# Performance work log

Measured on AMD Instinct MI355X. Metric: run time of the kernel, lower is better.

Reference implementation:

```python
import jax, jax.numpy as jnp
import numpy as np

EMB = 32      # emb_size = input_size // 2
IN = 64       # input_size
H = 128       # hidden_size
OUT = 256     # output_size (byte vocab)
TEMP = 1e-3   # Decoder_lstm.temperature


def _bytes(x):
    # x: [N] nonneg int32 -> [N, 4] big-endian bytes (vectorized get_bytes_2d)
    shifts = jnp.array([24, 16, 8, 0], dtype=x.dtype)
    return (x[:, None] >> shifts) & 0xFF


def _embed4(tables, byts):
    # tables: [4, 256, EMB]; byts: [N, 4] -> [N, 4*EMB] (concat of 4 gathers)
    return jnp.concatenate([tables[i][byts[:, i]] for i in range(4)], axis=-1)


def _encoder(x, W, b):
    # Encoder: sigmoid(Linear(4*EMB -> EMB))
    return jax.nn.sigmoid(x @ W.T + b)


def _lstm(xs, h0, c0, W_ih, W_hh, b_ih, b_hh):
    # xs: [S, B, IN]; PyTorch gate order i, f, g, o
    def step(carry, x_t):
        h, c = carry
        g = x_t @ W_ih.T + b_ih + h @ W_hh.T + b_hh  # [B, 4H]
        i, f, gg, o = jnp.split(g, 4, axis=-1)
        c = jax.nn.sigmoid(f) * c + jax.nn.sigmoid(i) * jnp.tanh(gg)
        h = jax.nn.sigmoid(o) * jnp.tanh(c)
        return (h, c), None
    (hf, cf), _ = jax.lax.scan(step, (h0, c0), xs)
    return hf, cf


def reference(inp, h0, c0, pc_emb, addr_emb, enc_W, enc_b, W_ih, W_hh, b_ih, b_hh, dec_W, dec_b, fc1_W, fc1_b, fc2_W, fc2_b):
    b, s, _ = inp.shape
    pc = inp[:, :, 0].reshape(-1)
    ad = inp[:, :, 1].reshape(-1)
    # byte decomposition + embedding gather + TimeDistributed encoder MLP
    pc_e = _encoder(_embed4(pc_emb, _bytes(pc)), enc_W, enc_b).reshape(b, s, EMB)
    ad_e = _encoder(_embed4(addr_emb, _bytes(ad)), enc_W, enc_b).reshape(b, s, EMB)
    emb = jnp.concatenate([pc_e, ad_e], axis=-1)  # [b, s, IN]
    # deterministic surrogate for KDE sample mean (expected value of 200 KDE draws)
    dist = jnp.mean(emb, axis=1)  # [b, IN]
    hf, _ = _lstm(jnp.swapaxes(emb, 0, 1), h0[0], c0[0], W_ih, W_hh, b_ih, b_hh)
    h_n = hf[None]  # [1, b, H] == hidden_cell[0]
    # Decoder_lstm: 4 parallel linears + low-temperature softmax
    logits = jnp.einsum('xbh,koh->kxbo', h_n, dec_W) + dec_b[:, None, None, :]  # [4,1,b,OUT]
    probs = jax.nn.softmax(logits / TEMP, axis=-1)
    # get_freq_rec: probs @ embedding tables, encoder MLP, concat dist, small MLP
    be = jnp.einsum('kxbo,koe->xbke', probs, addr_emb).reshape(1, b, 4 * EMB)
    fe = _encoder(be, enc_W, enc_b)[0]  # [b, EMB]
    fr_in = jnp.concatenate([fe, dist], axis=-1)  # [b, 3*EMB]
    fr = jax.nn.sigmoid(jax.nn.relu(fr_in @ fc1_W.T + fc1_b) @ fc2_W.T + fc2_b)
    return probs, logits, fr[:, 0], fr[:, 1]


def setup_inputs() -> dict:
    ks = jax.random.split(jax.random.key(0), 18)
    B, S = 64, 2048
    g = lambda k, shp: 0.1 * jax.random.normal(k, shp, dtype=jnp.float32)
    return {
        'inp': jax.random.randint(ks[0], (B, S, 2), 0, 2147483647, dtype=jnp.int32),
        'h0': g(ks[1], (1, B, H)),
        'c0': g(ks[2], (1, B, H)),
        'pc_emb': g(ks[3], (4, 256, EMB)),
        'addr_emb': g(ks[4], (4, 256, EMB)),
        'enc_W': g(ks[5], (EMB, 4 * EMB)),
        'enc_b': g(ks[6], (EMB,)),
        'W_ih': g(ks[7], (4 * H, IN)),
        'W_hh': g(ks[8], (4 * H, H)),
        'b_ih': g(ks[9], (4 * H,)),
        'b_hh': g(ks[10], (4 * H,)),
        'dec_W': g(ks[11], (4, OUT, H)),
        'dec_b': g(ks[12], (4, OUT)),
        'fc1_W': g(ks[13], (10, 3 * EMB)),
        'fc1_b': g(ks[14], (10,)),
        'fc2_W': g(ks[15], (2, 10)),
        'fc2_b': g(ks[16], (2,)),
    }
```

## Files before the change

kernel.cpp:

```cpp
#include <hip/hip_runtime.h>
#include <math.h>
#include <stdint.h>

#define EMBS 32
#define INS 64
#define HS 128
#define OUTS 256
#define BS 64
#define SS 2048

typedef _Float16 half2v __attribute__((ext_vector_type(2)));

static constexpr size_t WS_DIST  = (size_t)BS * SS * INS;
static constexpr size_t WS_HFIN  = WS_DIST + (size_t)BS * INS;
static constexpr size_t WS_XW    = WS_HFIN + (size_t)BS * HS;
static constexpr size_t WS_SMALL = WS_XW;
static constexpr size_t WS_BIG   = WS_XW + (size_t)BS * SS * 256;

__device__ __forceinline__ float fexp2(float x) {
#if __has_builtin(__builtin_amdgcn_exp2f)
    return __builtin_amdgcn_exp2f(x);
#else
    return exp2f(x);
#endif
}
__device__ __forceinline__ float frcp(float x) {
#if __has_builtin(__builtin_amdgcn_rcpf)
    return __builtin_amdgcn_rcpf(x);
#else
    return 1.f / x;
#endif
}
__device__ __forceinline__ float sigm(float x)  { return frcp(1.f + fexp2(-1.44269504f * x)); }
__device__ __forceinline__ float ftanh(float x) { return 1.f - 2.f * frcp(1.f + fexp2(2.88539008f * x)); }

__device__ __forceinline__ float fdot2f(half2v a, half2v b, float c) {
#if __has_builtin(__builtin_amdgcn_fdot2)
    return __builtin_amdgcn_fdot2(a, b, c, false);
#else
    return c + (float)a.x * (float)b.x + (float)a.y * (float)b.y;
#endif
}

__device__ __forceinline__ half2v pack2(float a, float b) {
    half2v r; r.x = (_Float16)a; r.y = (_Float16)b; return r;
}

__device__ __forceinline__ void gate_map(int tid, int& u, bool& lo, int& g0, int& g1) {
    int l = tid & 63;
    u = ((tid >> 6) << 5) + (l & 31);
    lo = (l < 32);
    g0 = lo ? u : 128 + u;
    g1 = lo ? 256 + u : 384 + u;
}

__global__ __launch_bounds__(256) void k_embed(
    const int* __restrict__ inp, const float* __restrict__ pc_emb,
    const float* __restrict__ ad_emb, const float* __restrict__ encW,
    const float* __restrict__ encB, float* __restrict__ emb)
{
    int idx = blockIdx.x * 256 + threadIdx.x;
    int b = idx >> 11, t = idx & 2047;
    size_t base = (size_t)b * SS + t;
    int2 pa = ((const int2*)inp)[base];
    float* outp = emb + base * INS;

    float in[128];
    #pragma unroll
    for (int st = 0; st < 2; st++) {
        int v = (st == 0) ? pa.x : pa.y;
        const float* tbl = (st == 0) ? pc_emb : ad_emb;
        #pragma unroll
        for (int i = 0; i < 4; i++) {
            int by = (v >> (24 - 8 * i)) & 255;
            const float4* row = (const float4*)(tbl + ((size_t)i * 256 + by) * EMBS);
            #pragma unroll
            for (int k = 0; k < 8; k++) {
                float4 f = row[k];
                in[i * 32 + k * 4 + 0] = f.x;
                in[i * 32 + k * 4 + 1] = f.y;
                in[i * 32 + k * 4 + 2] = f.z;
                in[i * 32 + k * 4 + 3] = f.w;
            }
        }
        for (int e = 0; e < EMBS; e++) {
            const float* w = encW + e * 128;
            float acc = encB[e];
            #pragma unroll
            for (int k = 0; k < 128; k++) acc += in[k] * w[k];
            outp[st * EMBS + e] = sigm(acc);
        }
    }
}

__global__ __launch_bounds__(256) void k_dist(const float* __restrict__ emb,
                                              float* __restrict__ dist)
{
    int b = blockIdx.x;
    int j = threadIdx.x & 63;
    int grp = threadIdx.x >> 6;
    float s = 0.f;
    for (int t = grp; t < SS; t += 4) s += emb[((size_t)b * SS + t) * INS + j];
    __shared__ float red[4][64];
    red[grp][j] = s;
    __syncthreads();
    if (grp == 0)
        dist[b * 64 + j] = (red[0][j] + red[1][j] + red[2][j] + red[3][j]) * (1.f / SS);
}

#define XW_ROWS 64
__global__ __launch_bounds__(256) void k_xw(
    const float* __restrict__ emb, const float* __restrict__ Wih,
    const float* __restrict__ bih, const float* __restrict__ bhh,
    half2v* __restrict__ xwv)
{
    int tid = threadIdx.x;
    size_t r0 = (size_t)blockIdx.x * XW_ROWS;
    int u, g0, g1; bool lo;
    gate_map(tid, u, lo, g0, g1);

    half2v wa[32], wb[32];
    const float* pa_ = Wih + (size_t)g0 * INS;
    const float* pb_ = Wih + (size_t)g1 * INS;
    #pragma unroll
    for (int i = 0; i < 32; i++) {
        wa[i] = pack2(pa_[2 * i], pa_[2 * i + 1]);
        wb[i] = pack2(pb_[2 * i], pb_[2 * i + 1]);
    }
    float ba = bih[g0] + bhh[g0], bb = bih[g1] + bhh[g1];

    __shared__ alignas(16) half2v xsh[XW_ROWS * 32];
    const float4* src = (const float4*)(emb + r0 * INS);
    #pragma unroll
    for (int k = 0; k < 4; k++) {
        int fi = k * 256 + tid;
        float4 v = src[fi];
        xsh[fi * 2]     = pack2(v.x, v.y);
        xsh[fi * 2 + 1] = pack2(v.z, v.w);
    }
    __syncthreads();

    #pragma unroll 2
    for (int r = 0; r < XW_ROWS; r++) {
        const half2v* xr = &xsh[r * 32];
        float a0 = 0.f, a1 = 0.f, b0 = 0.f, b1 = 0.f;
        #pragma unroll
        for (int i = 0; i < 32; i += 2) {
            half2v x0 = xr[i], x1 = xr[i + 1];
            a0 = fdot2f(x0, wa[i], a0);
            a1 = fdot2f(x1, wa[i + 1], a1);
            b0 = fdot2f(x0, wb[i], b0);
            b1 = fdot2f(x1, wb[i + 1], b1);
        }
        xwv[(r0 + r) * 256 + tid] = pack2(ba + a0 + a1, bb + b0 + b1);
    }
}

__global__ __launch_bounds__(256, 1) void k_lstm6(
    const half2v* __restrict__ xw, const float* __restrict__ h0,
    const float* __restrict__ c0, const float* __restrict__ Whh,
    float* __restrict__ hfin)
{
    int b = blockIdx.x;
    int tid = threadIdx.x;
    int u, g0_, g1_; bool lo;
    gate_map(tid, u, lo, g0_, g1_);
    int koff = lo ? 0 : 64;
    int kv   = lo ? 0 : 32;

    half2v wI[32], wF[32], wG[32], wO[32];
    {
        const float* rI = Whh + (size_t)(u)       * HS + koff;
        const float* rF = Whh + (size_t)(128 + u) * HS + koff;
        const float* rG = Whh + (size_t)(256 + u) * HS + koff;
        const float* rO = Whh + (size_t)(384 + u) * HS + koff;
        #pragma unroll
        for (int i = 0; i < 32; i++) {
            wI[i] = pack2(rI[2 * i], rI[2 * i + 1]);
            wF[i] = pack2(rF[2 * i], rF[2 * i + 1]);
            wG[i] = pack2(rG[2 * i], rG[2 * i + 1]);
            wO[i] = pack2(rO[2 * i], rO[2 * i + 1]);
        }
    }

    __shared__ alignas(16) _Float16 hsh[2][HS];
    float c = 0.f, h = 0.f;
    if (!lo) c = c0[b * HS + u];
    if (tid < 128) hsh[0][tid] = (_Float16)h0[b * HS + tid];
    __syncthreads();

    const half2v* xwrow = xw + (size_t)b * SS * 256 + tid;
    half2v xb0 = xwrow[0];
    half2v xb1 = xwrow[256];
    half2v xb2 = xwrow[512];
    half2v xb3 = xwrow[768];

#define LSTEP(XB, RB, TN)                                                      \
    {                                                                          \
        const half2v* hb = (const half2v*)hsh[RB] + kv;                        \
        half2v hr[32];                                                         \
        _Pragma("unroll")                                                      \
        for (int j_ = 0; j_ < 32; j_++) hr[j_] = hb[j_];                       \
        float pI = 0.f, pF = 0.f, pG = 0.f, pO = 0.f;                          \
        _Pragma("unroll")                                                      \
        for (int j_ = 0; j_ < 32; j_++) {                                      \
            half2v hv = hr[j_];                                                \
            pI = fdot2f(hv, wI[j_], pI);                                       \
            pF = fdot2f(hv, wF[j_], pF);                                       \
            pG = fdot2f(hv, wG[j_], pG);                                       \
            pO = fdot2f(hv, wO[j_], pO);                                       \
        }                                                                      \
                \
        float r1 = __shfl_xor(lo ? pF : pI, 32, 64); \
        float r2 = __shfl_xor(lo ? pO : pG, 32, 64); \
        float pre0 = (lo ? pI : pF) + r1 + (float)XB.x;                        \
        float pre1 = (lo ? pG : pO) + r2 + (float)XB.y;                        \
        float act0 = sigm(pre0);                            \
        float act1 = lo ? ftanh(pre1) : sigm(pre1);         \
        float pig = __shfl_xor(act0 * act1, 32, 64);      \
        if (!lo) {                                                             \
            c = __builtin_fmaf(act0, c, pig);                                  \
            h = act1 * ftanh(c);                                               \
            hsh[RB ^ 1][u] = (_Float16)h;                                      \
        }                                                                      \
        {                                                                      \
            int tn_ = (TN) < SS ? (TN) : (SS - 1);                             \
            XB = xwrow[(size_t)tn_ * 256];                                     \
        }                                                                      \
        asm volatile("s_waitcnt lgkmcnt(0)" ::: "memory");                     \
        __builtin_amdgcn_s_barrier();                                          \
        __builtin_amdgcn_sched_barrier(0);                                     \
    }

    for (int t = 0; t < SS; t += 4) {
        LSTEP(xb0, 0, t + 4)
        LSTEP(xb1, 1, t + 5)
        LSTEP(xb2, 0, t + 6)
        LSTEP(xb3, 1, t + 7)
    }
#undef LSTEP

    if (!lo) hfin[b * HS + u] = h;
}

__global__ __launch_bounds__(256, 1) void k_lstm_fb(
    const float* __restrict__ emb, const float* __restrict__ h0,
    const float* __restrict__ c0, const float* __restrict__ Wih,
    const float* __restrict__ Whh, const float* __restrict__ bih,
    const float* __restrict__ bhh, float* __restrict__ hfin)
{
    int b = blockIdx.x;
    int tid = threadIdx.x;

    half2v wih[2][32], whh[2][64];
    #pragma unroll
    for (int g = 0; g < 2; g++) {
        int gg = tid + g * 256;
        const float* wr = Wih + (size_t)gg * INS;
        #pragma unroll
        for (int i = 0; i < 32; i++) wih[g][i] = pack2(wr[2 * i], wr[2 * i + 1]);
        const float* hr = Whh + (size_t)gg * HS;
        #pragma unroll
        for (int i = 0; i < 64; i++) whh[g][i] = pack2(hr[2 * i], hr[2 * i + 1]);
    }
    float bias0 = bih[tid] + bhh[tid];
    float bias1 = bih[tid + 256] + bhh[tid + 256];

    __shared__ alignas(16) half2v xh[96];
    __shared__ float f_act[128], o_act[128];
    __shared__ float xf[64], hf[128];

    float c = 0.f, h = 0.f;
    if (tid < 128) c = c0[b * HS + tid];

    const float* xrow = emb + (size_t)b * SS * INS;
    if (tid < 64) xf[tid] = xrow[tid];
    if (tid < 128) hf[tid] = h0[b * HS + tid];
    __syncthreads();
    if (tid < 32) xh[tid] = pack2(xf[2 * tid], xf[2 * tid + 1]);
    else if (tid < 96) { int uu = tid - 32; xh[tid] = pack2(hf[2 * uu], hf[2 * uu + 1]); }
    __syncthreads();

    for (int t = 0; t < SS; t++) {
        float xn = 0.f;
        if (tid >= 128 && tid < 192 && t + 1 < SS) xn = xrow[(size_t)(t + 1) * INS + (tid - 128)];

        float a0a = 0.f, a0b = 0.f, a1a = 0.f, a1b = 0.f;
        #pragma unroll
        for (int i = 0; i < 32; i += 2) {
            half2v x0 = xh[i], x1 = xh[i + 1];
            a0a = fdot2f(x0, wih[0][i], a0a);
            a0b = fdot2f(x1, wih[0][i + 1], a0b);
            a1a = fdot2f(x0, wih[1][i], a1a);
            a1b = fdot2f(x1, wih[1][i + 1], a1b);
        }
        #pragma unroll
        for (int i = 0; i < 64; i += 2) {
            half2v h0v = xh[32 + i], h1v = xh[32 + i + 1];
            a0a = fdot2f(h0v, whh[0][i], a0a);
            a0b = fdot2f(h1v, whh[0][i + 1], a0b);
            a1a = fdot2f(h0v, whh[1][i], a1a);
            a1b = fdot2f(h1v, whh[1][i + 1], a1b);
        }
        float a0 = bias0 + a0a + a0b;
        float a1 = bias1 + a1a + a1b;

        float iact = 0.f, gact = 0.f;
        if (tid < 128) { iact = sigm(a0); gact = ftanh(a1); }
        else           { f_act[tid - 128] = sigm(a0); o_act[tid - 128] = sigm(a1); }
        __syncthreads();

        if (tid < 128) {
            c = f_act[tid] * c + iact * gact;
            h = o_act[tid] * ftanh(c);
            hf[tid] = h;
        } else if (tid < 192) {
            xf[tid - 128] = xn;
        }
        __syncthreads();

        if (tid < 32) xh[tid] = pack2(xf[2 * tid], xf[2 * tid + 1]);
        else if (tid < 96) { int uu = tid - 32; xh[tid] = pack2(hf[2 * uu], hf[2 * uu + 1]); }
        __syncthreads();
    }
    if (tid < 128) hfin[b * HS + tid] = h;
}

__global__ __launch_bounds__(256) void k_head(
    const float* __restrict__ hfin, const float* __restrict__ decW,
    const float* __restrict__ decB, const float* __restrict__ ad_emb,
    const float* __restrict__ encW, const float* __restrict__ encB,
    const float* __restrict__ dist, const float* __restrict__ fc1W,
    const float* __restrict__ fc1b, const float* __restrict__ fc2W,
    const float* __restrict__ fc2b, float* __restrict__ outp)
{
    int b = blockIdx.x;
    int tid = threadIdx.x;
    __shared__ float hsh[128];
    __shared__ float logit_s[4][256];
    __shared__ float probs_s[4][256];
    __shared__ float be_s[128];
    __shared__ float fe_dist[96];
    __shared__ float fr1[10];

    if (tid < 128) hsh[tid] = hfin[b * HS + tid];
    __syncthreads();

    #pragma unroll
    for (int k = 0; k < 4; k++) {
        const float* w = decW + ((size_t)k * OUTS + tid) * HS;
        float acc = decB[k * OUTS + tid];
        #pragma unroll 8
        for (int hh = 0; hh < HS; hh++) acc += hsh[hh] * w[hh];
        logit_s[k][tid] = acc;
        outp[65536 + k * 16384 + b * 256 + tid] = acc;
    }
    __syncthreads();

    {
        int k = tid >> 6, lane = tid & 63;
        float v0 = logit_s[k][lane],       v1 = logit_s[k][lane + 64];
        float v2 = logit_s[k][lane + 128], v3 = logit_s[k][lane + 192];
        float m = fmaxf(fmaxf(v0, v1), fmaxf(v2, v3));
        for (int off = 32; off; off >>= 1) m = fmaxf(m, __shfl_xor(m, off, 64));
        float e0 = fexp2((v0 - m) * 1442.695041f), e1 = fexp2((v1 - m) * 1442.695041f);
        float e2 = fexp2((v2 - m) * 1442.695041f), e3 = fexp2((v3 - m) * 1442.695041f);
        float s = e0 + e1 + e2 + e3;
        for (int off = 32; off; off >>= 1) s += __shfl_xor(s, off, 64);
        float inv = 1.f / s;
        float p0 = e0 * inv, p1 = e1 * inv, p2 = e2 * inv, p3 = e3 * inv;
        probs_s[k][lane] = p0;        probs_s[k][lane + 64] = p1;
        probs_s[k][lane + 128] = p2;  probs_s[k][lane + 192] = p3;
        outp[k * 16384 + b * 256 + lane] = p0;
        outp[k * 16384 + b * 256 + lane + 64] = p1;
        outp[k * 16384 + b * 256 + lane + 128] = p2;
        outp[k * 16384 + b * 256 + lane + 192] = p3;
    }
    __syncthreads();

    if (tid < 128) {
        int k = tid >> 5, e = tid & 31;
        const float* te = ad_emb + (size_t)k * OUTS * EMBS + e;
        float acc = 0.f;
        #pragma unroll 8
        for (int o = 0; o < OUTS; o++) acc += probs_s[k][o] * te[o * EMBS];
        be_s[tid] = acc;
    }
    __syncthreads();

    if (tid < 32) {
        const float* w = encW + tid * 128;
        float acc = encB[tid];
        #pragma unroll 8
        for (int kk = 0; kk < 128; kk++) acc += be_s[kk] * w[kk];
        fe_dist[tid] = sigm(acc);
    } else if (tid < 96) {
        fe_dist[tid] = dist[b * 64 + (tid - 32)];
    }
    __syncthreads();

    if (tid < 10) {
        float acc = fc1b[tid];
        for (int kk = 0; kk < 96; kk++) acc += fe_dist[kk] * fc1W[tid * 96 + kk];
        fr1[tid] = fmaxf(acc, 0.f);
    }
    __syncthreads();

    if (tid < 2) {
        float acc = fc2b[tid];
        for (int kk = 0; kk < 10; kk++) acc += fr1[kk] * fc2W[tid * 10 + kk];
        outp[131072 + tid * 64 + b] = sigm(acc);
    }
}

extern "C" void kernel_launch(void* const* d_in, const int* in_sizes, int n_in,
                              void* d_out, int out_size, void* d_ws, size_t ws_size,
                              hipStream_t stream)
{
    const int*   inp    = (const int*)d_in[0];
    const float* h0     = (const float*)d_in[1];
    const float* c0     = (const float*)d_in[2];
    const float* pc_emb = (const float*)d_in[3];
    const float* ad_emb = (const float*)d_in[4];
    const float* encW   = (const float*)d_in[5];
    const float* encB   = (const float*)d_in[6];
    const float* Wih    = (const float*)d_in[7];
    const float* Whh    = (const float*)d_in[8];
    const float* bih    = (const float*)d_in[9];
    const float* bhh    = (const float*)d_in[10];
    const float* decW   = (const float*)d_in[11];
    const float* decB   = (const float*)d_in[12];
    const float* fc1W   = (const float*)d_in[13];
    const float* fc1b   = (const float*)d_in[14];
    const float* fc2W   = (const float*)d_in[15];
    const float* fc2b   = (const float*)d_in[16];

    if (ws_size < WS_SMALL * 4ull) return;

    float* ws   = (float*)d_ws;
    float* emb  = ws;
    float* dist = ws + WS_DIST;
    float* hfin = ws + WS_HFIN;
    float* outp = (float*)d_out;
    bool big = (ws_size >= WS_BIG * 4ull);

    hipLaunchKernelGGL(k_embed, dim3(512), dim3(256), 0, stream,
                       inp, pc_emb, ad_emb, encW, encB, emb);
    hipLaunchKernelGGL(k_dist, dim3(64), dim3(256), 0, stream, emb, dist);
    if (big) {
        half2v* xwv = (half2v*)(ws + WS_XW);
        hipLaunchKernelGGL(k_xw, dim3(BS * SS / XW_ROWS), dim3(256), 0, stream,
                           emb, Wih, bih, bhh, xwv);
        hipLaunchKernelGGL(k_lstm6, dim3(64), dim3(256), 0, stream,
                           xwv, h0, c0, Whh, hfin);
    } else {
        hipLaunchKernelGGL(k_lstm_fb, dim3(64), dim3(256), 0, stream,
                           emb, h0, c0, Wih, Whh, bih, bhh, hfin);
    }
    hipLaunchKernelGGL(k_head, dim3(64), dim3(256), 0, stream,
                       hfin, decW, decB, ad_emb, encW, encB, dist,
                       fc1W, fc1b, fc2W, fc2b, outp);
}
```

Baseline: 1.497 ms.

## Compute LSTM recurrent matvec with MFMA 16x16x32 instead of dot2

Each time step's W_hh·h product now runs as MFMA 16x16x32 f16 instructions. Each wave holds a 128-row slice of W_hh as A fragments in registers, and the hidden state is broadcast as the B operand. The gate pre-activations are written to a shared-memory array and read back after an extra barrier, replacing the shuffle-based reduction. The goal is to cut the per-step dot-product issue cost on the serial critical path. In exchange it adds an extra LDS round trip and barrier per step, and MFMA latency on a dependency chain. Only one of the 16 output columns carries useful data.

```diff
diff --git a/kernel.cpp b/kernel.cpp
--- a/kernel.cpp
+++ b/kernel.cpp
@@ -10,6 +10,8 @@
 #define SS 2048
 
 typedef _Float16 half2v __attribute__((ext_vector_type(2)));
+typedef _Float16 half8 __attribute__((ext_vector_type(8)));
+typedef float f32x4 __attribute__((ext_vector_type(4)));
 
 static constexpr size_t WS_DIST  = (size_t)BS * SS * INS;
 static constexpr size_t WS_HFIN  = WS_DIST + (size_t)BS * INS;
@@ -156,34 +158,37 @@
     }
 }
 
-__global__ __launch_bounds__(256, 1) void k_lstm6(
+__global__ __launch_bounds__(256, 1) void k_lstm7(
     const half2v* __restrict__ xw, const float* __restrict__ h0,
     const float* __restrict__ c0, const float* __restrict__ Whh,
     float* __restrict__ hfin)
 {
     int b = blockIdx.x;
     int tid = threadIdx.x;
-    int u, g0_, g1_; bool lo;
-    gate_map(tid, u, lo, g0_, g1_);
-    int koff = lo ? 0 : 64;
-    int kv   = lo ? 0 : 32;
-
-    half2v wI[32], wF[32], wG[32], wO[32];
-    {
-        const float* rI = Whh + (size_t)(u)       * HS + koff;
-        const float* rF = Whh + (size_t)(128 + u) * HS + koff;
-        const float* rG = Whh + (size_t)(256 + u) * HS + koff;
-        const float* rO = Whh + (size_t)(384 + u) * HS + koff;
-        #pragma unroll
-        for (int i = 0; i < 32; i++) {
-            wI[i] = pack2(rI[2 * i], rI[2 * i + 1]);
-            wF[i] = pack2(rF[2 * i], rF[2 * i + 1]);
-            wG[i] = pack2(rG[2 * i], rG[2 * i + 1]);
-            wO[i] = pack2(rO[2 * i], rO[2 * i + 1]);
+    int w = tid >> 6;
+    int l = tid & 63;
+    int lrow = l & 15;
+    int lgrp = l >> 4;
+
+    int u, tg0, tg1; bool lo;
+    gate_map(tid, u, lo, tg0, tg1);
+
+    half8 wA[8][4];
+    #pragma unroll
+    for (int m = 0; m < 8; m++) {
+        #pragma unroll
+        for (int kt = 0; kt < 4; kt++) {
+            const float* src = Whh + (size_t)(w * 128 + m * 16 + lrow) * HS + kt * 32 + lgrp * 8;
+            half8 v;
+            #pragma unroll
+            for (int j = 0; j < 8; j++) v[j] = (_Float16)src[j];
+            wA[m][kt] = v;
         }
     }
 
     __shared__ alignas(16) _Float16 hsh[2][HS];
+    __shared__ alignas(16) float gates[512];
+
     float c = 0.f, h = 0.f;
     if (!lo) c = c0[b * HS + u];
     if (tid < 128) hsh[0][tid] = (_Float16)h0[b * HS + tid];
@@ -195,26 +200,35 @@
     half2v xb2 = xwrow[512];
     half2v xb3 = xwrow[768];
 
+    const f32x4 zero4 = {0.f, 0.f, 0.f, 0.f};
+
 #define LSTEP(XB, RB, TN)                                                      \
     {                                                                          \
-        const half2v* hb = (const half2v*)hsh[RB] + kv;                        \
-        half2v hr[32];                                                         \
+         \
+        const half8* hb = (const half8*)hsh[RB];                               \
+        half8 bf0 = hb[lgrp];                                                  \
+        half8 bf1 = hb[4 + lgrp];                                              \
+        half8 bf2 = hb[8 + lgrp];                                              \
+        half8 bf3 = hb[12 + lgrp];                                             \
+        f32x4 acc[8];                                                          \
         _Pragma("unroll")                                                      \
-        for (int j_ = 0; j_ < 32; j_++) hr[j_] = hb[j_];                       \
-        float pI = 0.f, pF = 0.f, pG = 0.f, pO = 0.f;                          \
+        for (int m_ = 0; m_ < 8; m_++) {                                       \
+            acc[m_] = __builtin_amdgcn_mfma_f32_16x16x32_f16(wA[m_][0], bf0, zero4, 0, 0, 0); \
+            acc[m_] = __builtin_amdgcn_mfma_f32_16x16x32_f16(wA[m_][1], bf1, acc[m_], 0, 0, 0); \
+            acc[m_] = __builtin_amdgcn_mfma_f32_16x16x32_f16(wA[m_][2], bf2, acc[m_], 0, 0, 0); \
+            acc[m_] = __builtin_amdgcn_mfma_f32_16x16x32_f16(wA[m_][3], bf3, acc[m_], 0, 0, 0); \
+        }                                                                      \
+               \
         _Pragma("unroll")                                                      \
-        for (int j_ = 0; j_ < 32; j_++) {                                      \
-            half2v hv = hr[j_];                                                \
-            pI = fdot2f(hv, wI[j_], pI);                                       \
-            pF = fdot2f(hv, wF[j_], pF);                                       \
-            pG = fdot2f(hv, wG[j_], pG);                                       \
-            pO = fdot2f(hv, wO[j_], pO);                                       \
-        }                                                                      \
-                \
-        float r1 = __shfl_xor(lo ? pF : pI, 32, 64); \
-        float r2 = __shfl_xor(lo ? pO : pG, 32, 64); \
-        float pre0 = (lo ? pI : pF) + r1 + (float)XB.x;                        \
-        float pre1 = (lo ? pG : pO) + r2 + (float)XB.y;                        \
+        for (int m_ = 0; m_ < 8; m_++)                                         \
+            if (lrow == m_)                                                    \
+                *(f32x4*)&gates[w * 128 + m_ * 16 + lgrp * 4] = acc[m_];       \
+        asm volatile("s_waitcnt lgkmcnt(0)" ::: "memory");                     \
+        __builtin_amdgcn_s_barrier();                                          \
+        __builtin_amdgcn_sched_barrier(0);                                     \
+                    \
+        float pre0 = gates[tg0] + (float)XB.x;                                 \
+        float pre1 = gates[tg1] + (float)XB.y;                                 \
         float act0 = sigm(pre0);                            \
         float act1 = lo ? ftanh(pre1) : sigm(pre1);         \
         float pig = __shfl_xor(act0 * act1, 32, 64);      \
@@ -451,7 +465,7 @@
         half2v* xwv = (half2v*)(ws + WS_XW);
         hipLaunchKernelGGL(k_xw, dim3(BS * SS / XW_ROWS), dim3(256), 0, stream,
                            emb, Wih, bih, bhh, xwv);
-        hipLaunchKernelGGL(k_lstm6, dim3(64), dim3(256), 0, stream,
+        hipLaunchKernelGGL(k_lstm7, dim3(64), dim3(256), 0, stream,
                            xwv, h0, c0, Whh, hfin);
     } else {
         hipLaunchKernelGGL(k_lstm_fb, dim3(64), dim3(256), 0, stream,
```

Result: slower. 1.821 ms (+21.6%).
